# Performance work log

Hardware: AMD Instinct MI355X
Metric: run time of the kernel (lower is better)

Reference implementation:

```python
import jax, jax.numpy as jnp
import numpy as np

MAX_OUTPUT = 25
SHARPNESS = 10.0

def soft_clamp(x, min_val, max_val, sharpness=SHARPNESS):
    x_norm = (x - min_val) / (max_val - min_val + 1e-06)
    x_clamped = jax.nn.sigmoid(sharpness * (x_norm - 0.5))
    return min_val + x_clamped * (max_val - min_val)

def setup_inputs() -> dict:
    key = jax.random.key(0)
    k1, = jax.random.split(key, 1)
    T = 2_000_000
    input_seq = jax.random.randint(k1, (T,), 0, 2, dtype=jnp.int32)
    # learned parameters, matching torch init values
    delta = jnp.array([0.5, -0.5], dtype=jnp.float32)
    out_scale = jnp.array(5.0, dtype=jnp.float32)
    return {"delta": delta, "out_scale": out_scale, "input_seq": input_seq}

def reference(delta, out_scale, input_seq):
    # counter_t = sum_{i<=t} delta[input_seq[i]]  (clamped value is NOT fed back,
    # so the recurrence is an exact cumulative sum)
    steps = delta[input_seq]                       # [T]
    counter = jnp.cumsum(steps)                    # [T]
    counter_soft = soft_clamp(counter, 0.0, float(MAX_OUTPUT - 1))  # [T]
    positions = jnp.arange(MAX_OUTPUT, dtype=counter_soft.dtype)    # [25]
    distances = jnp.abs(positions[None, :] - counter_soft[:, None]) # [T, 25]
    logits = -distances * out_scale
    return jax.nn.softmax(logits, axis=-1)         # [T, 25]
```

## Files before the change

kernel.cpp:

```cpp
#include <hip/hip_runtime.h>
#include <hip/hip_bf16.h>

#define MAXO 25
#define WCHUNK 512
#define BCHUNK 2048

__global__ __launch_bounds__(256) void pda_sums(
    const int* __restrict__ seq, unsigned* __restrict__ blk_sums, int T)
{
    __shared__ unsigned ws[4];
    const int lane = threadIdx.x & 63;
    const int wid  = threadIdx.x >> 6;

    const long t0 = (long)blockIdx.x * BCHUNK + (long)wid * WCHUNK + (long)lane * 8;
    unsigned s = 0;
    if (t0 + 8 <= (long)T) {
        const int4* p = (const int4*)(seq + t0);
        int4 a = p[0], b = p[1];
        s = (unsigned)(a.x + a.y + a.z + a.w + b.x + b.y + b.z + b.w);
    } else {
        for (int k = 0; k < 8; ++k) {
            long t = t0 + k;
            if (t < (long)T) s += (unsigned)seq[t];
        }
    }
    #pragma unroll
    for (int off = 32; off; off >>= 1) s += __shfl_down(s, off, 64);
    if (lane == 0) ws[wid] = s;
    __syncthreads();
    if (threadIdx.x == 0)
        blk_sums[blockIdx.x] = ws[0] + ws[1] + ws[2] + ws[3];
}

__global__ __launch_bounds__(256) void pda_main(
    const int* __restrict__ seq, const unsigned* __restrict__ blk_sums,
    const float* __restrict__ delta, const float* __restrict__ scale_p,
    float* __restrict__ out, int T)
{
    __shared__ __align__(16) float stage[4][64 * MAXO];
    __shared__ unsigned wsum[4];
    __shared__ unsigned bpart[4];

    const int lane = threadIdx.x & 63;
    const int wid  = threadIdx.x >> 6;
    const int bid  = blockIdx.x;
    const long wbase = (long)bid * BCHUNK + (long)wid * WCHUNK;

    const float d0 = delta[0];
    const float dd = delta[1] - d0;
    const float scale = scale_p[0];
    const float inv_denom = 1.0f / (24.0f + 1e-6f);

    unsigned long long m[8];
    unsigned mycnt = 0;
    #pragma unroll
    for (int r = 0; r < 8; ++r) {
        long t = wbase + (long)r * 64 + lane;
        int b = (t < (long)T) ? seq[t] : 0;
        m[r] = __ballot(b != 0);
        mycnt += (unsigned)__popcll(m[r]);
    }
    if (lane == 0) wsum[wid] = mycnt;

    unsigned p = 0;
    for (int i = (int)threadIdx.x; i < bid; i += 256) p += blk_sums[i];
    #pragma unroll
    for (int off = 32; off; off >>= 1) p += __shfl_down(p, off, 64);
    if (lane == 0) bpart[wid] = p;
    __syncthreads();

    unsigned run = bpart[0] + bpart[1] + bpart[2] + bpart[3];
    for (int w = 0; w < wid; ++w) run += wsum[w];

    const unsigned long long le_mask = (lane == 63) ? ~0ULL : ((2ULL << lane) - 1ULL);

    for (int r = 0; r < 8; ++r) {
        const long rbase = wbase + (long)r * 64;
        const long t = rbase + lane;

        unsigned ones_incl = run + (unsigned)__popcll(m[r] & le_mask);

        float c   = (float)(t + 1) * d0 + (float)ones_incl * dd;
        float z   = 10.0f * (c * inv_denom - 0.5f);
        float sig = 1.0f / (1.0f + __expf(-z));
        float cs  = sig * 24.0f;

        float w[MAXO];
        float sum = 0.0f;
        #pragma unroll
        for (int j = 0; j < MAXO; ++j) {
            float dist = fabsf((float)j - cs);
            w[j] = __expf(-scale * dist);
            sum += w[j];
        }
        float inv = 1.0f / sum;

        #pragma unroll
        for (int j = 0; j < MAXO; ++j)
            stage[wid][lane * MAXO + j] = w[j] * inv;

        long rem = (long)T - rbase;
        int V = (rem >= 64) ? 64 : (rem < 0 ? 0 : (int)rem);

        if (V == 64) {
            float4* o4 = (float4*)(out + rbase * MAXO);
            const float4* s4 = (const float4*)&stage[wid][0];
            #pragma unroll
            for (int s = 0; s < 6; ++s)
                o4[s * 64 + lane] = s4[s * 64 + lane];
            if (lane < 16) o4[384 + lane] = s4[384 + lane];
        } else if (V > 0) {
            int F = V * MAXO;
            for (int f = lane; f < F; f += 64)
                out[rbase * MAXO + f] = stage[wid][f];
        }

        run += (unsigned)__popcll(m[r]);
    }
}

extern "C" void kernel_launch(void* const* d_in, const int* in_sizes, int n_in,
                              void* d_out, int out_size, void* d_ws, size_t ws_size,
                              hipStream_t stream)
{
    const float* delta   = (const float*)d_in[0];
    const float* scale_p = (const float*)d_in[1];
    const int*   seq     = (const int*)d_in[2];
    const int T = in_sizes[2];
    const int nblocks = (T + BCHUNK - 1) / BCHUNK;

    unsigned* blk_sums = (unsigned*)d_ws;

    pda_sums<<<nblocks, 256, 0, stream>>>(seq, blk_sums, T);
    pda_main<<<nblocks, 256, 0, stream>>>(seq, blk_sums, delta, scale_p,
                                          (float*)d_out, T);
}
```

Baseline: 42.95 us.

## Replace two-pass block-sum scan with single-pass decoupled lookback

Merges the separate block-sum kernel and the main kernel into one kernel that publishes per-block aggregate and inclusive flags and resolves its exclusive prefix with a warp-parallel decoupled lookback. This removes one kernel launch, a full extra read of the input sequence, and the O(bid) per-block summation of all prior block sums. In exchange it adds a memset of the flag array, spin-waiting on predecessor blocks that assumes blocks are scheduled in order, and a launch-bounds occupancy hint.

```diff
diff --git a/kernel.cpp b/kernel.cpp
--- a/kernel.cpp
+++ b/kernel.cpp
@@ -5,51 +5,23 @@
 #define WCHUNK 512
 #define BCHUNK 2048
 
-__global__ __launch_bounds__(256) void pda_sums(
-    const int* __restrict__ seq, unsigned* __restrict__ blk_sums, int T)
-{
-    __shared__ unsigned ws[4];
-    const int lane = threadIdx.x & 63;
-    const int wid  = threadIdx.x >> 6;
+#define FLAG_AGG (1u << 30)
+#define FLAG_INC (2u << 30)
+#define FLAG_VAL 0x3FFFFFFFu
 
-    const long t0 = (long)blockIdx.x * BCHUNK + (long)wid * WCHUNK + (long)lane * 8;
-    unsigned s = 0;
-    if (t0 + 8 <= (long)T) {
-        const int4* p = (const int4*)(seq + t0);
-        int4 a = p[0], b = p[1];
-        s = (unsigned)(a.x + a.y + a.z + a.w + b.x + b.y + b.z + b.w);
-    } else {
-        for (int k = 0; k < 8; ++k) {
-            long t = t0 + k;
-            if (t < (long)T) s += (unsigned)seq[t];
-        }
-    }
-    #pragma unroll
-    for (int off = 32; off; off >>= 1) s += __shfl_down(s, off, 64);
-    if (lane == 0) ws[wid] = s;
-    __syncthreads();
-    if (threadIdx.x == 0)
-        blk_sums[blockIdx.x] = ws[0] + ws[1] + ws[2] + ws[3];
-}
-
-__global__ __launch_bounds__(256) void pda_main(
-    const int* __restrict__ seq, const unsigned* __restrict__ blk_sums,
+__global__ __launch_bounds__(256, 4) void pda_lookback(
+    const int* __restrict__ seq, unsigned* __restrict__ flags,
     const float* __restrict__ delta, const float* __restrict__ scale_p,
     float* __restrict__ out, int T)
 {
     __shared__ __align__(16) float stage[4][64 * MAXO];
     __shared__ unsigned wsum[4];
-    __shared__ unsigned bpart[4];
+    __shared__ unsigned s_excl;
 
     const int lane = threadIdx.x & 63;
     const int wid  = threadIdx.x >> 6;
     const int bid  = blockIdx.x;
     const long wbase = (long)bid * BCHUNK + (long)wid * WCHUNK;
-
-    const float d0 = delta[0];
-    const float dd = delta[1] - d0;
-    const float scale = scale_p[0];
-    const float inv_denom = 1.0f / (24.0f + 1e-6f);
 
     unsigned long long m[8];
     unsigned mycnt = 0;
@@ -61,15 +33,64 @@
         mycnt += (unsigned)__popcll(m[r]);
     }
     if (lane == 0) wsum[wid] = mycnt;
-
-    unsigned p = 0;
-    for (int i = (int)threadIdx.x; i < bid; i += 256) p += blk_sums[i];
-    #pragma unroll
-    for (int off = 32; off; off >>= 1) p += __shfl_down(p, off, 64);
-    if (lane == 0) bpart[wid] = p;
     __syncthreads();
 
-    unsigned run = bpart[0] + bpart[1] + bpart[2] + bpart[3];
+    const unsigned bsum = wsum[0] + wsum[1] + wsum[2] + wsum[3];
+
+    if (threadIdx.x == 0) {
+        unsigned tag = (bid == 0) ? FLAG_INC : FLAG_AGG;
+        __hip_atomic_store(&flags[bid], tag | bsum, __ATOMIC_RELEASE,
+                           __HIP_MEMORY_SCOPE_AGENT);
+    }
+
+    if (wid == 0) {
+        unsigned excl = 0;
+        if (bid > 0) {
+            int j = bid - 1;
+            for (;;) {
+                int  idx = j - lane;
+                bool vl  = (idx >= 0);
+                unsigned f;
+                do {
+                    f = vl ? __hip_atomic_load(&flags[idx], __ATOMIC_ACQUIRE,
+                                               __HIP_MEMORY_SCOPE_AGENT)
+                           : 0u;
+                } while (__any(vl && f == 0u));
+
+                unsigned long long inc_mask = __ballot(vl && (f >> 30) == 2u);
+                unsigned contrib;
+                bool done;
+                if (inc_mask) {
+                    int flead = (int)(__ffsll((long long)inc_mask) - 1);
+                    contrib = (vl && lane <= flead) ? (f & FLAG_VAL) : 0u;
+                    done = true;
+                } else {
+                    contrib = vl ? (f & FLAG_VAL) : 0u;
+                    done = false;
+                }
+                #pragma unroll
+                for (int off = 32; off; off >>= 1)
+                    contrib += __shfl_down(contrib, off, 64);
+                excl += __shfl(contrib, 0, 64);
+
+                if (done) break;
+                j -= 64;
+                if (j < 0) break;
+            }
+            if (lane == 0)
+                __hip_atomic_store(&flags[bid], FLAG_INC | (excl + bsum),
+                                   __ATOMIC_RELEASE, __HIP_MEMORY_SCOPE_AGENT);
+        }
+        if (lane == 0) s_excl = excl;
+    }
+    __syncthreads();
+
+    const float d0 = delta[0];
+    const float dd = delta[1] - d0;
+    const float scale = scale_p[0];
+    const float inv_denom = 1.0f / (24.0f + 1e-6f);
+
+    unsigned run = s_excl;
     for (int w = 0; w < wid; ++w) run += wsum[w];
 
     const unsigned long long le_mask = (lane == 63) ? ~0ULL : ((2ULL << lane) - 1ULL);
@@ -129,9 +150,9 @@
     const int T = in_sizes[2];
     const int nblocks = (T + BCHUNK - 1) / BCHUNK;
 
-    unsigned* blk_sums = (unsigned*)d_ws;
+    unsigned* flags = (unsigned*)d_ws;
 
-    pda_sums<<<nblocks, 256, 0, stream>>>(seq, blk_sums, T);
-    pda_main<<<nblocks, 256, 0, stream>>>(seq, blk_sums, delta, scale_p,
-                                          (float*)d_out, T);
+    hipMemsetAsync(flags, 0, (size_t)nblocks * sizeof(unsigned), stream);
+    pda_lookback<<<nblocks, 256, 0, stream>>>(seq, flags, delta, scale_p,
+                                              (float*)d_out, T);
 }
```

After: 114.1 us. 166% more time.

## Pack input bits into masks in first pass and use per-wave prefix sums

Applied to the files above, without the earlier changes.

The first pass now packs each wave's 512 binary inputs into eight 64-bit masks and writes per-wave popcounts. The main kernel reads these compact masks instead of re-reading the int32 sequence. It also computes its prefix per wave without block-level shared memory or a barrier. The aim is to cut the main kernel's input traffic. The cost is a longer serial prefix scan over four times as many partial sums per wave.

```diff
diff --git a/kernel.cpp b/kernel.cpp
--- a/kernel.cpp
+++ b/kernel.cpp
@@ -5,72 +5,71 @@
 #define WCHUNK 512
 #define BCHUNK 2048
 
-__global__ __launch_bounds__(256) void pda_sums(
-    const int* __restrict__ seq, unsigned* __restrict__ blk_sums, int T)
+__global__ __launch_bounds__(256) void pda_pass1(
+    const int* __restrict__ seq, unsigned long long* __restrict__ masks,
+    unsigned* __restrict__ wave_sums, int T)
 {
-    __shared__ unsigned ws[4];
     const int lane = threadIdx.x & 63;
     const int wid  = threadIdx.x >> 6;
+    const int gwid = blockIdx.x * 4 + wid;
+    const long base = (long)gwid * WCHUNK + (long)lane * 8;
 
-    const long t0 = (long)blockIdx.x * BCHUNK + (long)wid * WCHUNK + (long)lane * 8;
-    unsigned s = 0;
-    if (t0 + 8 <= (long)T) {
-        const int4* p = (const int4*)(seq + t0);
-        int4 a = p[0], b = p[1];
-        s = (unsigned)(a.x + a.y + a.z + a.w + b.x + b.y + b.z + b.w);
+    unsigned byte = 0;
+    if (base + 8 <= (long)T) {
+        const int4* p4 = (const int4*)(seq + base);
+        int4 a = p4[0], b = p4[1];
+        byte =  (unsigned)(a.x & 1)        | ((unsigned)(a.y & 1) << 1)
+             | ((unsigned)(a.z & 1) << 2)  | ((unsigned)(a.w & 1) << 3)
+             | ((unsigned)(b.x & 1) << 4)  | ((unsigned)(b.y & 1) << 5)
+             | ((unsigned)(b.z & 1) << 6)  | ((unsigned)(b.w & 1) << 7);
     } else {
         for (int k = 0; k < 8; ++k) {
-            long t = t0 + k;
-            if (t < (long)T) s += (unsigned)seq[t];
+            long t = base + k;
+            if (t < (long)T) byte |= (unsigned)(seq[t] & 1) << k;
         }
     }
+
+    unsigned long long v = (unsigned long long)byte << ((lane & 7) * 8);
+    v |= __shfl_xor(v, 1, 64);
+    v |= __shfl_xor(v, 2, 64);
+    v |= __shfl_xor(v, 4, 64);
+    if ((lane & 7) == 0)
+        masks[(size_t)gwid * 8 + (lane >> 3)] = v;
+
+    unsigned s = __popc(byte);
     #pragma unroll
     for (int off = 32; off; off >>= 1) s += __shfl_down(s, off, 64);
-    if (lane == 0) ws[wid] = s;
-    __syncthreads();
-    if (threadIdx.x == 0)
-        blk_sums[blockIdx.x] = ws[0] + ws[1] + ws[2] + ws[3];
+    if (lane == 0) wave_sums[gwid] = s;
 }
 
 __global__ __launch_bounds__(256) void pda_main(
-    const int* __restrict__ seq, const unsigned* __restrict__ blk_sums,
+    const unsigned long long* __restrict__ masks,
+    const unsigned* __restrict__ wave_sums,
     const float* __restrict__ delta, const float* __restrict__ scale_p,
     float* __restrict__ out, int T)
 {
     __shared__ __align__(16) float stage[4][64 * MAXO];
-    __shared__ unsigned wsum[4];
-    __shared__ unsigned bpart[4];
 
     const int lane = threadIdx.x & 63;
     const int wid  = threadIdx.x >> 6;
-    const int bid  = blockIdx.x;
-    const long wbase = (long)bid * BCHUNK + (long)wid * WCHUNK;
+    const int gwid = blockIdx.x * 4 + wid;
+    const long wbase = (long)gwid * WCHUNK;
 
     const float d0 = delta[0];
     const float dd = delta[1] - d0;
     const float scale = scale_p[0];
     const float inv_denom = 1.0f / (24.0f + 1e-6f);
 
-    unsigned long long m[8];
-    unsigned mycnt = 0;
-    #pragma unroll
-    for (int r = 0; r < 8; ++r) {
-        long t = wbase + (long)r * 64 + lane;
-        int b = (t < (long)T) ? seq[t] : 0;
-        m[r] = __ballot(b != 0);
-        mycnt += (unsigned)__popcll(m[r]);
-    }
-    if (lane == 0) wsum[wid] = mycnt;
-
     unsigned p = 0;
-    for (int i = (int)threadIdx.x; i < bid; i += 256) p += blk_sums[i];
+    for (int i = lane; i < gwid; i += 64) p += wave_sums[i];
     #pragma unroll
     for (int off = 32; off; off >>= 1) p += __shfl_down(p, off, 64);
-    if (lane == 0) bpart[wid] = p;
-    __syncthreads();
+    unsigned run = __shfl(p, 0, 64);
 
-    unsigned run = bpart[0] + bpart[1] + bpart[2] + bpart[3];
-    for (int w = 0; w < wid; ++w) run += wsum[w];
+    unsigned long long m[8];
+    const unsigned long long* mp = masks + (size_t)gwid * 8;
+    #pragma unroll
+    for (int r = 0; r < 8; ++r) m[r] = mp[r];
 
     const unsigned long long le_mask = (lane == 63) ? ~0ULL : ((2ULL << lane) - 1ULL);
 
@@ -128,10 +127,12 @@
     const int*   seq     = (const int*)d_in[2];
     const int T = in_sizes[2];
     const int nblocks = (T + BCHUNK - 1) / BCHUNK;
+    const int nwaves  = nblocks * 4;
 
-    unsigned* blk_sums = (unsigned*)d_ws;
+    unsigned long long* masks = (unsigned long long*)d_ws;
+    unsigned* wave_sums = (unsigned*)(masks + (size_t)nwaves * 8);
 
-    pda_sums<<<nblocks, 256, 0, stream>>>(seq, blk_sums, T);
-    pda_main<<<nblocks, 256, 0, stream>>>(seq, blk_sums, delta, scale_p,
-                                          (float*)d_out, T);
+    pda_pass1<<<nblocks, 256, 0, stream>>>(seq, masks, wave_sums, T);
+    pda_main <<<nblocks, 256, 0, stream>>>(masks, wave_sums, delta, scale_p,
+                                           (float*)d_out, T);
 }
```

After: 43.98 us. 2.4% more time.
